# Kernel optimization log

Hardware: AMD Instinct MI355X
Metric: run time of the kernel (lower is better)

## Reference

```python
import jax, jax.numpy as jnp
import numpy as np

CONF_THRES = 0.25
IOU_THRES = 0.45
MAX_DET = 300
K_NMS = 2048          # static candidate cap for jit-compatible NMS
MAX_WH = 7680.0       # yolov5 class-offset trick for non-agnostic NMS
IN_H, IN_W = 640.0, 640.0     # network input size (self.size)
OUT_H, OUT_W = 1080.0, 1920.0  # original frame size (h, w)


def setup_inputs() -> dict:
    key = jax.random.key(0)
    k1, k2, k3, k4 = jax.random.split(key, 4)
    bs, n, nc = 16, 25200, 80
    # realistic raw yolov5 head output: xywh in pixels, obj/cls in [0,1]
    xy = jax.random.uniform(k1, (bs, n, 2), jnp.float32) * 640.0
    wh = jax.random.uniform(k2, (bs, n, 2), jnp.float32) * 120.0 + 2.0
    obj = jax.random.uniform(k3, (bs, n, 1), jnp.float32)
    cls = jax.random.uniform(k4, (bs, n, nc), jnp.float32)
    preds = jnp.concatenate([xy, wh, obj, cls], axis=-1)  # [bs, 25200, 85]
    return {"preds": preds}


def _xywh2xyxy(x):
    xy, wh = x[..., :2], x[..., 2:4]
    return jnp.concatenate([xy - wh * 0.5, xy + wh * 0.5], axis=-1)


def _iou_one_many(b, boxes):
    # b: [4], boxes: [K,4] (xyxy) -> [K]
    lt = jnp.maximum(b[:2], boxes[:, :2])
    rb = jnp.minimum(b[2:], boxes[:, 2:])
    wh = jnp.clip(rb - lt, 0.0)
    inter = wh[:, 0] * wh[:, 1]
    a1 = (b[2] - b[0]) * (b[3] - b[1])
    a2 = (boxes[:, 2] - boxes[:, 0]) * (boxes[:, 3] - boxes[:, 1])
    return inter / (a1 + a2 - inter + 1e-7)


def _nms_sorted(boxes, valid):
    # boxes [K,4] sorted by score desc (class-offset applied); valid [K] bool
    K = boxes.shape[0]
    idxs = jnp.arange(K)

    def step(suppressed, i):
        keep_i = valid[i] & jnp.logical_not(suppressed[i])
        iou = _iou_one_many(boxes[i], boxes)  # [K]
        suppressed = suppressed | (keep_i & (iou > IOU_THRES) & (idxs > i))
        return suppressed, keep_i

    _, keep = jax.lax.scan(step, jnp.zeros((K,), bool), idxs)
    # first MAX_DET kept indices (stable: preserves score order)
    sel = jnp.argsort(jnp.logical_not(keep), stable=True)[:MAX_DET]
    return sel, keep[sel]


def reference(preds):
    # --- yolov5 non_max_suppression (multi_label=False, agnostic=False) ---
    obj = preds[..., 4:5]                      # [bs,N,1]
    cls_conf = preds[..., 5:] * obj            # conf = obj * cls
    conf = jnp.max(cls_conf, axis=-1)          # [bs,N]
    cls = jnp.argmax(cls_conf, axis=-1)        # [bs,N] int
    mask = (preds[..., 4] > CONF_THRES) & (conf > CONF_THRES)
    score = jnp.where(mask, conf, -1.0)

    top_s, top_i = jax.lax.top_k(score, K_NMS)                      # [bs,K]
    cand_xywh = jnp.take_along_axis(preds[..., :4], top_i[..., None], axis=1)
    cand_boxes = _xywh2xyxy(cand_xywh)                              # [bs,K,4]
    cand_cls = jnp.take_along_axis(cls, top_i, axis=1)              # [bs,K]
    valid = top_s > 0.0

    boxes_off = cand_boxes + cand_cls[..., None].astype(cand_boxes.dtype) * MAX_WH
    sel, keep = jax.vmap(_nms_sorted)(boxes_off, valid)             # [bs,MAX_DET]

    det_boxes = jnp.take_along_axis(cand_boxes, sel[..., None], axis=1)
    det_scores = jnp.take_along_axis(top_s, sel, axis=1)
    det_cls = jnp.take_along_axis(cand_cls, sel, axis=1)

    # --- scale_bbox: (640,640) -> (h,w) original frame ---
    scale = jnp.array([OUT_W / IN_W, OUT_H / IN_H, OUT_W / IN_W, OUT_H / IN_H],
                      dtype=det_boxes.dtype)
    det_boxes = det_boxes * scale

    det = jnp.concatenate(
        [det_boxes, det_scores[..., None], det_cls[..., None].astype(det_boxes.dtype)],
        axis=-1)                                                    # [bs,MAX_DET,6]
    det = jnp.where(keep[..., None], det, 0.0)
    return det
```

## Files before the change

### kernel.cpp

```cpp
#include <hip/hip_runtime.h>
#include <stdint.h>

#define BS 16
#define NP 25200
#define NC 80
#define DIM 85
#define KN 2048
#define CAP 4096
#define BINS 512
#define MAXD 300
#define SBLK 99
#define QCAP 128

__global__ __launch_bounds__(256) void score_hist_kernel(const float* __restrict__ preds,
        float* __restrict__ score, int* __restrict__ clsout, int* __restrict__ hpart) {
    int b = blockIdx.x / SBLK;
    int chunk = blockIdx.x % SBLK;
    int tid = threadIdx.x;
    __shared__ int h[BINS];
    h[tid] = 0; h[tid + 256] = 0;
    __syncthreads();
    int n = chunk * 256 + tid;
    if (n < NP) {
        const float* bp = preds + ((size_t)b * NP + n) * DIM;
        float obj = bp[4];
        float sc = -1.0f; int bidx = 0;
        if (obj > 0.25f) {
            float best = -1.0f;
            #pragma unroll
            for (int kk = 0; kk < 10; ++kk) {
                float v[8];
                #pragma unroll
                for (int j = 0; j < 8; ++j) v[j] = bp[5 + kk * 8 + j];
                #pragma unroll
                for (int j = 0; j < 8; ++j) {
                    float s = v[j] * obj;
                    if (s > best) { best = s; bidx = kk * 8 + j; }
                }
            }
            if (best > 0.25f) sc = best;
        }
        int gi = b * NP + n;
        score[gi] = sc;
        clsout[gi] = bidx;
        if (sc > 0.0f) {
            int bin = (int)(__float_as_uint(sc) >> 15) - 0x7D00;
            bin = max(0, min(BINS - 1, bin));
            atomicAdd(&h[bin], 1);
        }
    }
    __syncthreads();
    int* hp = hpart + ((size_t)(b * SBLK + chunk)) * BINS;
    hp[tid] = h[tid];
    hp[tid + 256] = h[tid + 256];
}

template<int V, bool DESC, typename T>
__device__ inline void wave_bitonic(T (&v)[V], int lane) {
    const int N = V * 64;
    #pragma unroll
    for (int k = 2; k <= N; k <<= 1) {
        #pragma unroll
        for (int j = N >> 1; j > 0; j >>= 1) {
            if (j >= k) continue;
            if (j >= 64) {
                int dv = j >> 6;
                #pragma unroll
                for (int a = 0; a < V; ++a) {
                    int p = a ^ dv;
                    if (a < p) {
                        int e = a * 64;
                        bool kml = (((e & k) == 0) == DESC);
                        T lo = v[a], hi = v[p];
                        T mx = lo > hi ? lo : hi;
                        T mn = lo > hi ? hi : lo;
                        v[a] = kml ? mx : mn;
                        v[p] = kml ? mn : mx;
                    }
                }
            } else {
                #pragma unroll
                for (int a = 0; a < V; ++a) {
                    int e = a * 64 + lane;
                    T pv = __shfl_xor(v[a], j);
                    bool isLower = (lane & j) == 0;
                    bool kml = (((e & k) == 0) == DESC);
                    bool takeMax = (kml == isLower);
                    T mx = v[a] > pv ? v[a] : pv;
                    T mn = v[a] > pv ? pv : v[a];
                    v[a] = takeMax ? mx : mn;
                }
            }
        }
    }
}

__global__ __launch_bounds__(1024) void sort16_kernel(const float* __restrict__ score,
        const int* __restrict__ hpart,
        unsigned long long* __restrict__ gkeys, int* __restrict__ gmeta,
        int* __restrict__ gbstart, int* __restrict__ gcnt,
        unsigned char* __restrict__ carrU8, unsigned char* __restrict__ keepG) {
    int b = blockIdx.x;
    int tid = threadIdx.x;
    int lane = tid & 63;
    __shared__ int h[BINS];
    __shared__ int bstartA[BINS];
    __shared__ int bcnt[BINS];
    __shared__ int sT;
    if (tid < BINS) {
        int s = 0;
        const int* hp = hpart + ((size_t)b * SBLK) * BINS + tid;
        for (int c = 0; c < SBLK; ++c) s += hp[c * BINS];
        h[tid] = s;
        bcnt[tid] = 0;
    }
    __syncthreads();
    if (tid < 64) {
        int base = lane * 8;
        int v[8]; int ssum = 0;
        #pragma unroll
        for (int kk = 0; kk < 8; ++kk) { v[kk] = h[base + kk]; ssum += v[kk]; }
        int x = ssum;
        #pragma unroll
        for (int off = 1; off < 64; off <<= 1) {
            int y = __shfl_down(x, off);
            if (lane + off < 64) x += y;
        }
        int run = x - ssum;
        int cand = -1;
        #pragma unroll
        for (int kk = 7; kk >= 0; --kk) {
            bstartA[base + kk] = run;
            run += v[kk];
            if (run >= KN && cand < 0) cand = base + kk;
        }
        #pragma unroll
        for (int off = 1; off < 64; off <<= 1) cand = max(cand, __shfl_xor(cand, off));
        if (lane == 0) sT = max(cand, 0);
    }
    __syncthreads();
    int T = sT;
    int n = min(bstartA[T] + h[T], CAP);
    int Mb = min(n, KN);
    const float* sb = score + (size_t)b * NP;
    for (int i = tid; i < NP; i += 1024) {
        float sc = sb[i];
        if (sc > 0.0f) {
            int bin = (int)(__float_as_uint(sc) >> 15) - 0x7D00;
            bin = max(0, min(BINS - 1, bin));
            if (bin >= T) {
                int pos = bstartA[bin] + atomicAdd(&bcnt[bin], 1);
                if (pos < CAP) {
                    unsigned int ii = (unsigned int)i;
                    gkeys[(size_t)b * CAP + pos] =
                        ((unsigned long long)__float_as_uint(sc) << 32)
                        | (unsigned int)(~ii);
                }
            }
        }
    }
    for (int r = tid; r < KN; r += 1024) { keepG[b * KN + r] = 0; carrU8[b * KN + r] = 0xFF; }
    if (tid < BINS) { gbstart[b * BINS + tid] = bstartA[tid]; gcnt[b * BINS + tid] = h[tid]; }
    if (tid == 0) { gmeta[2 * b] = T; gmeta[2 * b + 1] = Mb; }
}

__global__ __launch_bounds__(256) void binsort_build_kernel(const float* __restrict__ preds,
        const int* __restrict__ cls, unsigned long long* __restrict__ gkeys,
        const int* __restrict__ gmeta, const int* __restrict__ gbstart,
        const int* __restrict__ gcnt,
        float4* __restrict__ gboxes, unsigned char* __restrict__ carrU8) {
    int b = blockIdx.x >> 5;
    int g = blockIdx.x & 31;
    int lane = threadIdx.x & 63;
    int wv = threadIdx.x >> 6;
    int T = gmeta[2 * b];
    int Mb = gmeta[2 * b + 1];
    int wslot = g * 4 + wv;
    for (int bin = T + wslot; bin < BINS; bin += 128) {
        int cnt = gcnt[b * BINS + bin];
        if (cnt <= 0) continue;
        int bs = gbstart[b * BINS + bin];
        if (bs >= Mb) continue;
        unsigned long long v[4];
        #pragma unroll
        for (int a = 0; a < 4; ++a) {
            int idx = a * 64 + lane;
            v[a] = (idx < cnt && bs + idx < CAP) ? gkeys[(size_t)b * CAP + bs + idx] : 0ull;
        }
        wave_bitonic<4, true>(v, lane);
        #pragma unroll
        for (int a = 0; a < 4; ++a) {
            int idx = a * 64 + lane;
            if (idx < cnt && bs + idx < CAP) gkeys[(size_t)b * CAP + bs + idx] = v[a];
        }
        #pragma unroll
        for (int a = 0; a < 4; ++a) {
            int idx = a * 64 + lane;
            int r = bs + idx;
            if (idx < cnt && r < Mb) {
                unsigned long long key = v[a];
                unsigned int i = ~(unsigned int)key;
                const float* p = preds + ((size_t)b * NP + i) * DIM;
                float x = p[0], y = p[1], w = p[2], hh = p[3];
                gboxes[b * KN + r] = make_float4(x - w * 0.5f, y - hh * 0.5f,
                                                x + w * 0.5f, y + hh * 0.5f);
                carrU8[b * KN + r] = (unsigned char)cls[(size_t)b * NP + i];
            }
        }
    }
}

__global__ __launch_bounds__(64) void nms_kernel(const float4* __restrict__ gboxes,
        const unsigned char* __restrict__ carrU8, const int* __restrict__ gmeta,
        unsigned char* __restrict__ keepG) {
    int b = blockIdx.x / NC;
    int c = blockIdx.x % NC;
    int lane = threadIdx.x;
    int Mb = gmeta[2 * b + 1];
    __shared__ unsigned short q[QCAP];
    int base = 0;
    for (int r0 = 0; r0 < Mb; r0 += 64) {
        int r = r0 + lane;
        bool mine = (r < Mb) && (carrU8[b * KN + r] == (unsigned char)c);
        unsigned long long m = __ballot(mine);
        int pos = base + (int)__popcll(m & ((1ull << lane) - 1ull));
        if (mine && pos < QCAP) q[pos] = (unsigned short)r;
        base += (int)__popcll(m);
    }
    __syncthreads();
    int nc = min(base, QCAP);
    if (nc <= 0) return;
    int ord0 = (lane < nc) ? (int)q[lane] : 0;
    int ord1 = (lane + 64 < nc) ? (int)q[64 + lane] : 0;
    float4 A0 = (lane < nc) ? gboxes[b * KN + ord0] : make_float4(0.f, 0.f, 0.f, 0.f);
    float4 A1 = (lane + 64 < nc) ? gboxes[b * KN + ord1] : make_float4(0.f, 0.f, 0.f, 0.f);
    float off = (float)c * 7680.0f;
    A0.x += off; A0.y += off; A0.z += off; A0.w += off;
    A1.x += off; A1.y += off; A1.z += off; A1.w += off;
    float ar0 = (A0.z - A0.x) * (A0.w - A0.y);
    float ar1 = (A1.z - A1.x) * (A1.w - A1.y);
    unsigned long long sup0 = 0, sup1 = 0, keep0 = 0, keep1 = 0;
    for (int idx = 0; idx < nc; ++idx) {
        bool hi = idx >= 64;
        int bit = idx & 63;
        unsigned long long s = hi ? sup1 : sup0;
        if ((s >> bit) & 1ull) continue;
        if (hi) keep1 |= 1ull << bit; else keep0 |= 1ull << bit;
        float bx_ = hi ? __shfl(A1.x, bit) : __shfl(A0.x, bit);
        float by_ = hi ? __shfl(A1.y, bit) : __shfl(A0.y, bit);
        float bz_ = hi ? __shfl(A1.z, bit) : __shfl(A0.z, bit);
        float bw_ = hi ? __shfl(A1.w, bit) : __shfl(A0.w, bit);
        float ba_ = hi ? __shfl(ar1, bit) : __shfl(ar0, bit);
        bool s0, s1;
        {
            float lx = fmaxf(bx_, A0.x), ly = fmaxf(by_, A0.y);
            float rx = fminf(bz_, A0.z), ry = fminf(bw_, A0.w);
            float iw = fmaxf(rx - lx, 0.0f), ih = fmaxf(ry - ly, 0.0f);
            float inter = iw * ih;
            float iou = inter / (ba_ + ar0 - inter + 1e-7f);
            s0 = (lane > idx) && (lane < nc) && (iou > 0.45f);
        }
        {
            float lx = fmaxf(bx_, A1.x), ly = fmaxf(by_, A1.y);
            float rx = fminf(bz_, A1.z), ry = fminf(bw_, A1.w);
            float iw = fmaxf(rx - lx, 0.0f), ih = fmaxf(ry - ly, 0.0f);
            float inter = iw * ih;
            float iou = inter / (ba_ + ar1 - inter + 1e-7f);
            s1 = ((64 + lane) > idx) && ((64 + lane) < nc) && (iou > 0.45f);
        }
        sup0 |= __ballot(s0);
        sup1 |= __ballot(s1);
    }
    if (lane < nc && ((keep0 >> lane) & 1ull)) keepG[b * KN + ord0] = 1;
    if (lane + 64 < nc && ((keep1 >> lane) & 1ull)) keepG[b * KN + ord1] = 1;
}

__global__ __launch_bounds__(64) void out_kernel(const unsigned char* __restrict__ keepG,
        const unsigned long long* __restrict__ gkeys, const float4* __restrict__ gboxes,
        const unsigned char* __restrict__ carrU8, float* __restrict__ out) {
    int b = blockIdx.x;
    int lane = threadIdx.x;
    int running = 0;
    for (int ch = 0; ch < 32; ++ch) {
        int r = ch * 64 + lane;
        bool kp = keepG[b * KN + r] != 0;
        unsigned long long m = __ballot(kp);
        int pos = running + (int)__popcll(m & ((1ull << lane) - 1ull));
        if (kp && pos < MAXD) {
            float4 bx = gboxes[b * KN + r];
            float sc = __uint_as_float((unsigned int)(gkeys[(size_t)b * CAP + r] >> 32));
            float* o = out + ((size_t)b * MAXD + pos) * 6;
            o[0] = bx.x * 3.0f;
            o[1] = bx.y * 1.6875f;
            o[2] = bx.z * 3.0f;
            o[3] = bx.w * 1.6875f;
            o[4] = sc;
            o[5] = (float)carrU8[b * KN + r];
        }
        running += (int)__popcll(m);
    }
}

extern "C" void kernel_launch(void* const* d_in, const int* in_sizes, int n_in,
                              void* d_out, int out_size, void* d_ws, size_t ws_size,
                              hipStream_t stream) {
    const float* preds = (const float*)d_in[0];
    float* out = (float*)d_out;
    char* ws = (char*)d_ws;
    size_t off = 0;
    auto alloc = [&](size_t bytes) -> void* {
        void* p = ws + off;
        off += (bytes + 255) & ~(size_t)255;
        return p;
    };
    float* score = (float*)alloc((size_t)BS * NP * 4);
    int* cls    = (int*)alloc((size_t)BS * NP * 4);
    int* hpart  = (int*)alloc((size_t)BS * SBLK * BINS * 4);
    unsigned long long* gkeys = (unsigned long long*)alloc((size_t)BS * CAP * 8);
    float4* gboxes = (float4*)alloc((size_t)BS * KN * 16);
    unsigned char* carrU8 = (unsigned char*)alloc((size_t)BS * KN);
    unsigned char* keepG  = (unsigned char*)alloc((size_t)BS * KN);
    int* gmeta   = (int*)alloc(BS * 2 * 4);
    int* gbstart = (int*)alloc((size_t)BS * BINS * 4);
    int* gcnt    = (int*)alloc((size_t)BS * BINS * 4);
    if (ws_size < off) return;

    hipMemsetAsync(d_out, 0, (size_t)out_size * 4, stream);

    score_hist_kernel<<<BS * SBLK, 256, 0, stream>>>(preds, score, cls, hpart);
    sort16_kernel<<<BS, 1024, 0, stream>>>(score, hpart, gkeys, gmeta, gbstart, gcnt,
                                           carrU8, keepG);
    binsort_build_kernel<<<BS * 32, 256, 0, stream>>>(preds, cls, gkeys, gmeta,
                                                      gbstart, gcnt, gboxes, carrU8);
    nms_kernel<<<BS * NC, 64, 0, stream>>>(gboxes, carrU8, gmeta, keepG);
    out_kernel<<<BS, 64, 0, stream>>>(keepG, gkeys, gboxes, carrU8, out);
}
```

Baseline: 262.5 us.

## Stage preds tiles through LDS and parallelize threshold scatter across blocks

The score/histogram kernel now loads contiguous 64-box tiles of preds into shared memory as coalesced float4 reads with double buffering, and splits each box's 80-class argmax across 4 lanes with shuffle reduction. The former single-block-per-batch sort16 kernel is split into a small threshold kernel, which also converts per-block histograms into per-block scatter offsets, and a 2048-block scatter kernel. This targets the uncoalesced strided preds reads and the serial 25200-element scan per batch, at the cost of one extra kernel launch and large shared-memory usage per block.

```diff
diff --git a/kernel.cpp b/kernel.cpp
--- a/kernel.cpp
+++ b/kernel.cpp
@@ -9,50 +9,180 @@
 #define CAP 4096
 #define BINS 512
 #define MAXD 300
-#define SBLK 99
+#define SCB 128
 #define QCAP 128
 
 __global__ __launch_bounds__(256) void score_hist_kernel(const float* __restrict__ preds,
         float* __restrict__ score, int* __restrict__ clsout, int* __restrict__ hpart) {
-    int b = blockIdx.x / SBLK;
-    int chunk = blockIdx.x % SBLK;
+    int b = blockIdx.x >> 7;
+    int blk = blockIdx.x & 127;
     int tid = threadIdx.x;
+    __shared__ float4 sbuf[2][1360];
     __shared__ int h[BINS];
     h[tid] = 0; h[tid + 256] = 0;
-    __syncthreads();
-    int n = chunk * 256 + tid;
-    if (n < NP) {
-        const float* bp = preds + ((size_t)b * NP + n) * DIM;
-        float obj = bp[4];
-        float sc = -1.0f; int bidx = 0;
-        if (obj > 0.25f) {
-            float best = -1.0f;
+    int g0  = (blk < 10) ? blk * 4 : blk * 3 + 10;
+    int cnt = (blk < 10) ? 4 : 3;
+    {
+        const float4* p4 = (const float4*)(preds + ((size_t)b * NP + (size_t)g0 * 64) * DIM);
+        int nb = min(64, NP - g0 * 64);
+        int tot4 = (nb * DIM) >> 2;
+        #pragma unroll
+        for (int kx = 0; kx < 6; ++kx) {
+            int idx = kx * 256 + tid;
+            if (idx < tot4) sbuf[0][idx] = p4[idx];
+        }
+    }
+    __syncthreads();
+    float4 tmp[6];
+    for (int i = 0; i < cnt; ++i) {
+        int tot4n = 0;
+        if (i + 1 < cnt) {
+            int g1 = g0 + i + 1;
+            int nb1 = min(64, NP - g1 * 64);
+            tot4n = (nb1 * DIM) >> 2;
+            const float4* p4 = (const float4*)(preds + ((size_t)b * NP + (size_t)g1 * 64) * DIM);
             #pragma unroll
-            for (int kk = 0; kk < 10; ++kk) {
-                float v[8];
-                #pragma unroll
-                for (int j = 0; j < 8; ++j) v[j] = bp[5 + kk * 8 + j];
-                #pragma unroll
-                for (int j = 0; j < 8; ++j) {
-                    float s = v[j] * obj;
-                    if (s > best) { best = s; bidx = kk * 8 + j; }
+            for (int kx = 0; kx < 6; ++kx) {
+                int idx = kx * 256 + tid;
+                tmp[kx] = (idx < tot4n) ? p4[idx] : make_float4(0.f, 0.f, 0.f, 0.f);
+            }
+        }
+        int gg = g0 + i;
+        int nb = min(64, NP - gg * 64);
+        const float* s = (const float*)sbuf[i & 1];
+        int box = tid >> 2, sub = tid & 3;
+        if (box < nb) {
+            const float* bp = s + box * DIM;
+            float obj = bp[4];
+            float best = -1.0f; int bidx = sub * 20;
+            #pragma unroll
+            for (int c = 0; c < 20; ++c) {
+                float v = bp[5 + sub * 20 + c] * obj;
+                if (v > best) { best = v; bidx = sub * 20 + c; }
+            }
+            #pragma unroll
+            for (int off = 1; off < 4; off <<= 1) {
+                float ob = __shfl_xor(best, off);
+                int   oi = __shfl_xor(bidx, off);
+                if (ob > best || (ob == best && oi < bidx)) { best = ob; bidx = oi; }
+            }
+            if (sub == 0) {
+                bool m = (obj > 0.25f) && (best > 0.25f);
+                float sc = m ? best : -1.0f;
+                int gidx = b * NP + gg * 64 + box;
+                score[gidx] = sc;
+                clsout[gidx] = bidx;
+                if (sc > 0.0f) {
+                    int bin = (int)(__float_as_uint(sc) >> 15) - 0x7D00;
+                    bin = max(0, min(BINS - 1, bin));
+                    atomicAdd(&h[bin], 1);
                 }
             }
-            if (best > 0.25f) sc = best;
-        }
-        int gi = b * NP + n;
-        score[gi] = sc;
-        clsout[gi] = bidx;
+        }
+        __syncthreads();
+        if (i + 1 < cnt) {
+            #pragma unroll
+            for (int kx = 0; kx < 6; ++kx) {
+                int idx = kx * 256 + tid;
+                if (idx < tot4n) sbuf[(i + 1) & 1][idx] = tmp[kx];
+            }
+            __syncthreads();
+        }
+    }
+    int* hp = hpart + ((size_t)(b * SCB + blk)) * BINS;
+    hp[tid] = h[tid];
+    hp[tid + 256] = h[tid + 256];
+}
+
+__global__ __launch_bounds__(512) void thresh_kernel(int* __restrict__ hpart,
+        int* __restrict__ gmeta, int* __restrict__ gbstart, int* __restrict__ gcnt,
+        unsigned char* __restrict__ carrU8, unsigned char* __restrict__ keepG) {
+    int b = blockIdx.x;
+    int tid = threadIdx.x;
+    int lane = tid & 63;
+    __shared__ int h[BINS];
+    __shared__ int bstartA[BINS];
+    __shared__ int sT;
+    int* hp = hpart + (size_t)b * SCB * BINS;
+    int s = 0;
+    for (int c = 0; c < SCB; ++c) s += hp[c * BINS + tid];
+    h[tid] = s;
+    __syncthreads();
+    if (tid < 64) {
+        int base = lane * 8;
+        int v[8]; int ssum = 0;
+        #pragma unroll
+        for (int kk = 0; kk < 8; ++kk) { v[kk] = h[base + kk]; ssum += v[kk]; }
+        int x = ssum;
+        #pragma unroll
+        for (int off = 1; off < 64; off <<= 1) {
+            int y = __shfl_down(x, off);
+            if (lane + off < 64) x += y;
+        }
+        int run = x - ssum;
+        int cand = -1;
+        #pragma unroll
+        for (int kk = 7; kk >= 0; --kk) {
+            bstartA[base + kk] = run;
+            run += v[kk];
+            if (run >= KN && cand < 0) cand = base + kk;
+        }
+        #pragma unroll
+        for (int off = 1; off < 64; off <<= 1) cand = max(cand, __shfl_xor(cand, off));
+        if (lane == 0) sT = max(cand, 0);
+    }
+    __syncthreads();
+    int T = sT;
+    int run = bstartA[tid];
+    for (int c = 0; c < SCB; ++c) {
+        int t = hp[c * BINS + tid];
+        hp[c * BINS + tid] = run;
+        run += t;
+    }
+    gbstart[b * BINS + tid] = bstartA[tid];
+    gcnt[b * BINS + tid] = h[tid];
+    if (tid == 0) {
+        int n = min(bstartA[T] + h[T], CAP);
+        gmeta[2 * b] = T;
+        gmeta[2 * b + 1] = min(n, KN);
+    }
+    for (int r = tid; r < KN; r += 512) { keepG[b * KN + r] = 0; carrU8[b * KN + r] = 0xFF; }
+}
+
+__global__ __launch_bounds__(256) void scatter_kernel(const float* __restrict__ score,
+        const int* __restrict__ hpart, const int* __restrict__ gmeta,
+        unsigned long long* __restrict__ gkeys) {
+    int b = blockIdx.x >> 7;
+    int blk = blockIdx.x & 127;
+    int tid = threadIdx.x;
+    __shared__ int basep[BINS];
+    __shared__ int cntL[BINS];
+    const int* hp = hpart + (size_t)(b * SCB + blk) * BINS;
+    basep[tid] = hp[tid]; basep[tid + 256] = hp[tid + 256];
+    cntL[tid] = 0; cntL[tid + 256] = 0;
+    __syncthreads();
+    int T = gmeta[2 * b];
+    int g0  = (blk < 10) ? blk * 4 : blk * 3 + 10;
+    int cntg = (blk < 10) ? 4 : 3;
+    int r0 = g0 * 64;
+    int nrows = min(cntg * 64, NP - r0);
+    for (int r = tid; r < nrows; r += 256) {
+        int i = r0 + r;
+        float sc = score[b * NP + i];
         if (sc > 0.0f) {
             int bin = (int)(__float_as_uint(sc) >> 15) - 0x7D00;
             bin = max(0, min(BINS - 1, bin));
-            atomicAdd(&h[bin], 1);
-        }
-    }
-    __syncthreads();
-    int* hp = hpart + ((size_t)(b * SBLK + chunk)) * BINS;
-    hp[tid] = h[tid];
-    hp[tid + 256] = h[tid + 256];
+            if (bin >= T) {
+                int pos = basep[bin] + atomicAdd(&cntL[bin], 1);
+                if (pos < CAP) {
+                    unsigned int ii = (unsigned int)i;
+                    gkeys[(size_t)b * CAP + pos] =
+                        ((unsigned long long)__float_as_uint(sc) << 32)
+                        | (unsigned int)(~ii);
+                }
+            }
+        }
+    }
 }
 
 template<int V, bool DESC, typename T>
@@ -93,75 +223,6 @@
             }
         }
     }
-}
-
-__global__ __launch_bounds__(1024) void sort16_kernel(const float* __restrict__ score,
-        const int* __restrict__ hpart,
-        unsigned long long* __restrict__ gkeys, int* __restrict__ gmeta,
-        int* __restrict__ gbstart, int* __restrict__ gcnt,
-        unsigned char* __restrict__ carrU8, unsigned char* __restrict__ keepG) {
-    int b = blockIdx.x;
-    int tid = threadIdx.x;
-    int lane = tid & 63;
-    __shared__ int h[BINS];
-    __shared__ int bstartA[BINS];
-    __shared__ int bcnt[BINS];
-    __shared__ int sT;
-    if (tid < BINS) {
-        int s = 0;
-        const int* hp = hpart + ((size_t)b * SBLK) * BINS + tid;
-        for (int c = 0; c < SBLK; ++c) s += hp[c * BINS];
-        h[tid] = s;
-        bcnt[tid] = 0;
-    }
-    __syncthreads();
-    if (tid < 64) {
-        int base = lane * 8;
-        int v[8]; int ssum = 0;
-        #pragma unroll
-        for (int kk = 0; kk < 8; ++kk) { v[kk] = h[base + kk]; ssum += v[kk]; }
-        int x = ssum;
-        #pragma unroll
-        for (int off = 1; off < 64; off <<= 1) {
-            int y = __shfl_down(x, off);
-            if (lane + off < 64) x += y;
-        }
-        int run = x - ssum;
-        int cand = -1;
-        #pragma unroll
-        for (int kk = 7; kk >= 0; --kk) {
-            bstartA[base + kk] = run;
-            run += v[kk];
-            if (run >= KN && cand < 0) cand = base + kk;
-        }
-        #pragma unroll
-        for (int off = 1; off < 64; off <<= 1) cand = max(cand, __shfl_xor(cand, off));
-        if (lane == 0) sT = max(cand, 0);
-    }
-    __syncthreads();
-    int T = sT;
-    int n = min(bstartA[T] + h[T], CAP);
-    int Mb = min(n, KN);
-    const float* sb = score + (size_t)b * NP;
-    for (int i = tid; i < NP; i += 1024) {
-        float sc = sb[i];
-        if (sc > 0.0f) {
-            int bin = (int)(__float_as_uint(sc) >> 15) - 0x7D00;
-            bin = max(0, min(BINS - 1, bin));
-            if (bin >= T) {
-                int pos = bstartA[bin] + atomicAdd(&bcnt[bin], 1);
-                if (pos < CAP) {
-                    unsigned int ii = (unsigned int)i;
-                    gkeys[(size_t)b * CAP + pos] =
-                        ((unsigned long long)__float_as_uint(sc) << 32)
-                        | (unsigned int)(~ii);
-                }
-            }
-        }
-    }
-    for (int r = tid; r < KN; r += 1024) { keepG[b * KN + r] = 0; carrU8[b * KN + r] = 0xFF; }
-    if (tid < BINS) { gbstart[b * BINS + tid] = bstartA[tid]; gcnt[b * BINS + tid] = h[tid]; }
-    if (tid == 0) { gmeta[2 * b] = T; gmeta[2 * b + 1] = Mb; }
 }
 
 __global__ __launch_bounds__(256) void binsort_build_kernel(const float* __restrict__ preds,
@@ -315,7 +376,7 @@
     };
     float* score = (float*)alloc((size_t)BS * NP * 4);
     int* cls    = (int*)alloc((size_t)BS * NP * 4);
-    int* hpart  = (int*)alloc((size_t)BS * SBLK * BINS * 4);
+    int* hpart  = (int*)alloc((size_t)BS * SCB * BINS * 4);
     unsigned long long* gkeys = (unsigned long long*)alloc((size_t)BS * CAP * 8);
     float4* gboxes = (float4*)alloc((size_t)BS * KN * 16);
     unsigned char* carrU8 = (unsigned char*)alloc((size_t)BS * KN);
@@ -327,9 +388,9 @@
 
     hipMemsetAsync(d_out, 0, (size_t)out_size * 4, stream);
 
-    score_hist_kernel<<<BS * SBLK, 256, 0, stream>>>(preds, score, cls, hpart);
-    sort16_kernel<<<BS, 1024, 0, stream>>>(score, hpart, gkeys, gmeta, gbstart, gcnt,
-                                           carrU8, keepG);
+    score_hist_kernel<<<BS * SCB, 256, 0, stream>>>(preds, score, cls, hpart);
+    thresh_kernel<<<BS, 512, 0, stream>>>(hpart, gmeta, gbstart, gcnt, carrU8, keepG);
+    scatter_kernel<<<BS * SCB, 256, 0, stream>>>(score, hpart, gmeta, gkeys);
     binsort_build_kernel<<<BS * 32, 256, 0, stream>>>(preds, cls, gkeys, gmeta,
                                                       gbstart, gcnt, gboxes, carrU8);
     nms_kernel<<<BS * NC, 64, 0, stream>>>(gboxes, carrU8, gmeta, keepG);
```

New measurement: 256.9 us. -2.1%, faster.

## Fuse sort, box build, NMS and output into one per-batch LDS kernel

Applied to the files above, without the earlier changes.

Four per-batch kernels (bin scatter, per-bin bitonic sort plus box gather, per-class NMS, output compaction) become one 1024-thread block per image. All keys, boxes, classes and keep flags now live in shared memory. Each of the 16 waves handles five classes' NMS in turn. The separate memset of the output is dropped; the kernel zeroes only the unused tail rows. This removes several launches and the global-memory round trips between stages. In exchange, binsort and NMS run on 16 blocks instead of hundreds, so much less of the GPU is used during those phases, and the block needs a large LDS footprint.

```diff
diff --git a/kernel.cpp b/kernel.cpp
--- a/kernel.cpp
+++ b/kernel.cpp
@@ -95,25 +95,32 @@
     }
 }
 
-__global__ __launch_bounds__(1024) void sort16_kernel(const float* __restrict__ score,
-        const int* __restrict__ hpart,
-        unsigned long long* __restrict__ gkeys, int* __restrict__ gmeta,
-        int* __restrict__ gbstart, int* __restrict__ gcnt,
-        unsigned char* __restrict__ carrU8, unsigned char* __restrict__ keepG) {
+__global__ __launch_bounds__(1024) void tail_kernel(const float* __restrict__ score,
+        const float* __restrict__ preds, const int* __restrict__ cls,
+        const int* __restrict__ hpart, float* __restrict__ out) {
     int b = blockIdx.x;
     int tid = threadIdx.x;
     int lane = tid & 63;
+    int wid = tid >> 6;
+
+    __shared__ unsigned long long k[CAP];
+    __shared__ float4 bx4[KN];
+    __shared__ unsigned char carr[KN];
+    __shared__ unsigned char keep[KN];
+    __shared__ unsigned short q[16][QCAP];
     __shared__ int h[BINS];
     __shared__ int bstartA[BINS];
     __shared__ int bcnt[BINS];
-    __shared__ int sT;
+    __shared__ int sT, sMb, sKept;
+
     if (tid < BINS) {
         int s = 0;
-        const int* hp = hpart + ((size_t)b * SBLK) * BINS + tid;
+        const int* hp = hpart + (size_t)b * SBLK * BINS + tid;
         for (int c = 0; c < SBLK; ++c) s += hp[c * BINS];
         h[tid] = s;
         bcnt[tid] = 0;
     }
+    for (int r = tid; r < KN; r += 1024) { carr[r] = 0xFF; keep[r] = 0; }
     __syncthreads();
     if (tid < 64) {
         int base = lane * 8;
@@ -139,9 +146,14 @@
         if (lane == 0) sT = max(cand, 0);
     }
     __syncthreads();
+    if (tid == 0) {
+        int T = sT;
+        int n = min(bstartA[T] + h[T], CAP);
+        sMb = min(n, KN);
+    }
+    __syncthreads();
     int T = sT;
-    int n = min(bstartA[T] + h[T], CAP);
-    int Mb = min(n, KN);
+    int Mb = sMb;
     const float* sb = score + (size_t)b * NP;
     for (int i = tid; i < NP; i += 1024) {
         float sc = sb[i];
@@ -152,46 +164,29 @@
                 int pos = bstartA[bin] + atomicAdd(&bcnt[bin], 1);
                 if (pos < CAP) {
                     unsigned int ii = (unsigned int)i;
-                    gkeys[(size_t)b * CAP + pos] =
-                        ((unsigned long long)__float_as_uint(sc) << 32)
-                        | (unsigned int)(~ii);
+                    k[pos] = ((unsigned long long)__float_as_uint(sc) << 32)
+                           | (unsigned int)(~ii);
                 }
             }
         }
     }
-    for (int r = tid; r < KN; r += 1024) { keepG[b * KN + r] = 0; carrU8[b * KN + r] = 0xFF; }
-    if (tid < BINS) { gbstart[b * BINS + tid] = bstartA[tid]; gcnt[b * BINS + tid] = h[tid]; }
-    if (tid == 0) { gmeta[2 * b] = T; gmeta[2 * b + 1] = Mb; }
-}
-
-__global__ __launch_bounds__(256) void binsort_build_kernel(const float* __restrict__ preds,
-        const int* __restrict__ cls, unsigned long long* __restrict__ gkeys,
-        const int* __restrict__ gmeta, const int* __restrict__ gbstart,
-        const int* __restrict__ gcnt,
-        float4* __restrict__ gboxes, unsigned char* __restrict__ carrU8) {
-    int b = blockIdx.x >> 5;
-    int g = blockIdx.x & 31;
-    int lane = threadIdx.x & 63;
-    int wv = threadIdx.x >> 6;
-    int T = gmeta[2 * b];
-    int Mb = gmeta[2 * b + 1];
-    int wslot = g * 4 + wv;
-    for (int bin = T + wslot; bin < BINS; bin += 128) {
-        int cnt = gcnt[b * BINS + bin];
+    __syncthreads();
+    for (int bin = T + wid; bin < BINS; bin += 16) {
+        int cnt = h[bin];
         if (cnt <= 0) continue;
-        int bs = gbstart[b * BINS + bin];
+        int bs = bstartA[bin];
         if (bs >= Mb) continue;
         unsigned long long v[4];
         #pragma unroll
         for (int a = 0; a < 4; ++a) {
             int idx = a * 64 + lane;
-            v[a] = (idx < cnt && bs + idx < CAP) ? gkeys[(size_t)b * CAP + bs + idx] : 0ull;
+            v[a] = (idx < cnt && bs + idx < CAP) ? k[bs + idx] : 0ull;
         }
         wave_bitonic<4, true>(v, lane);
         #pragma unroll
         for (int a = 0; a < 4; ++a) {
             int idx = a * 64 + lane;
-            if (idx < cnt && bs + idx < CAP) gkeys[(size_t)b * CAP + bs + idx] = v[a];
+            if (idx < cnt && bs + idx < CAP) k[bs + idx] = v[a];
         }
         #pragma unroll
         for (int a = 0; a < 4; ++a) {
@@ -202,103 +197,100 @@
                 unsigned int i = ~(unsigned int)key;
                 const float* p = preds + ((size_t)b * NP + i) * DIM;
                 float x = p[0], y = p[1], w = p[2], hh = p[3];
-                gboxes[b * KN + r] = make_float4(x - w * 0.5f, y - hh * 0.5f,
-                                                x + w * 0.5f, y + hh * 0.5f);
-                carrU8[b * KN + r] = (unsigned char)cls[(size_t)b * NP + i];
-            }
-        }
-    }
-}
-
-__global__ __launch_bounds__(64) void nms_kernel(const float4* __restrict__ gboxes,
-        const unsigned char* __restrict__ carrU8, const int* __restrict__ gmeta,
-        unsigned char* __restrict__ keepG) {
-    int b = blockIdx.x / NC;
-    int c = blockIdx.x % NC;
-    int lane = threadIdx.x;
-    int Mb = gmeta[2 * b + 1];
-    __shared__ unsigned short q[QCAP];
-    int base = 0;
-    for (int r0 = 0; r0 < Mb; r0 += 64) {
-        int r = r0 + lane;
-        bool mine = (r < Mb) && (carrU8[b * KN + r] == (unsigned char)c);
-        unsigned long long m = __ballot(mine);
-        int pos = base + (int)__popcll(m & ((1ull << lane) - 1ull));
-        if (mine && pos < QCAP) q[pos] = (unsigned short)r;
-        base += (int)__popcll(m);
-    }
-    __syncthreads();
-    int nc = min(base, QCAP);
-    if (nc <= 0) return;
-    int ord0 = (lane < nc) ? (int)q[lane] : 0;
-    int ord1 = (lane + 64 < nc) ? (int)q[64 + lane] : 0;
-    float4 A0 = (lane < nc) ? gboxes[b * KN + ord0] : make_float4(0.f, 0.f, 0.f, 0.f);
-    float4 A1 = (lane + 64 < nc) ? gboxes[b * KN + ord1] : make_float4(0.f, 0.f, 0.f, 0.f);
-    float off = (float)c * 7680.0f;
-    A0.x += off; A0.y += off; A0.z += off; A0.w += off;
-    A1.x += off; A1.y += off; A1.z += off; A1.w += off;
-    float ar0 = (A0.z - A0.x) * (A0.w - A0.y);
-    float ar1 = (A1.z - A1.x) * (A1.w - A1.y);
-    unsigned long long sup0 = 0, sup1 = 0, keep0 = 0, keep1 = 0;
-    for (int idx = 0; idx < nc; ++idx) {
-        bool hi = idx >= 64;
-        int bit = idx & 63;
-        unsigned long long s = hi ? sup1 : sup0;
-        if ((s >> bit) & 1ull) continue;
-        if (hi) keep1 |= 1ull << bit; else keep0 |= 1ull << bit;
-        float bx_ = hi ? __shfl(A1.x, bit) : __shfl(A0.x, bit);
-        float by_ = hi ? __shfl(A1.y, bit) : __shfl(A0.y, bit);
-        float bz_ = hi ? __shfl(A1.z, bit) : __shfl(A0.z, bit);
-        float bw_ = hi ? __shfl(A1.w, bit) : __shfl(A0.w, bit);
-        float ba_ = hi ? __shfl(ar1, bit) : __shfl(ar0, bit);
-        bool s0, s1;
-        {
-            float lx = fmaxf(bx_, A0.x), ly = fmaxf(by_, A0.y);
-            float rx = fminf(bz_, A0.z), ry = fminf(bw_, A0.w);
-            float iw = fmaxf(rx - lx, 0.0f), ih = fmaxf(ry - ly, 0.0f);
-            float inter = iw * ih;
-            float iou = inter / (ba_ + ar0 - inter + 1e-7f);
-            s0 = (lane > idx) && (lane < nc) && (iou > 0.45f);
-        }
-        {
-            float lx = fmaxf(bx_, A1.x), ly = fmaxf(by_, A1.y);
-            float rx = fminf(bz_, A1.z), ry = fminf(bw_, A1.w);
-            float iw = fmaxf(rx - lx, 0.0f), ih = fmaxf(ry - ly, 0.0f);
-            float inter = iw * ih;
-            float iou = inter / (ba_ + ar1 - inter + 1e-7f);
-            s1 = ((64 + lane) > idx) && ((64 + lane) < nc) && (iou > 0.45f);
-        }
-        sup0 |= __ballot(s0);
-        sup1 |= __ballot(s1);
-    }
-    if (lane < nc && ((keep0 >> lane) & 1ull)) keepG[b * KN + ord0] = 1;
-    if (lane + 64 < nc && ((keep1 >> lane) & 1ull)) keepG[b * KN + ord1] = 1;
-}
-
-__global__ __launch_bounds__(64) void out_kernel(const unsigned char* __restrict__ keepG,
-        const unsigned long long* __restrict__ gkeys, const float4* __restrict__ gboxes,
-        const unsigned char* __restrict__ carrU8, float* __restrict__ out) {
-    int b = blockIdx.x;
-    int lane = threadIdx.x;
-    int running = 0;
-    for (int ch = 0; ch < 32; ++ch) {
-        int r = ch * 64 + lane;
-        bool kp = keepG[b * KN + r] != 0;
-        unsigned long long m = __ballot(kp);
-        int pos = running + (int)__popcll(m & ((1ull << lane) - 1ull));
-        if (kp && pos < MAXD) {
-            float4 bx = gboxes[b * KN + r];
-            float sc = __uint_as_float((unsigned int)(gkeys[(size_t)b * CAP + r] >> 32));
-            float* o = out + ((size_t)b * MAXD + pos) * 6;
-            o[0] = bx.x * 3.0f;
-            o[1] = bx.y * 1.6875f;
-            o[2] = bx.z * 3.0f;
-            o[3] = bx.w * 1.6875f;
-            o[4] = sc;
-            o[5] = (float)carrU8[b * KN + r];
-        }
-        running += (int)__popcll(m);
-    }
+                bx4[r] = make_float4(x - w * 0.5f, y - hh * 0.5f,
+                                     x + w * 0.5f, y + hh * 0.5f);
+                carr[r] = (unsigned char)cls[(size_t)b * NP + i];
+            }
+        }
+    }
+    __syncthreads();
+    #pragma unroll
+    for (int t5 = 0; t5 < 5; ++t5) {
+        int c = wid + 16 * t5;
+        unsigned short* qw = q[wid];
+        int base = 0;
+        for (int r0 = 0; r0 < Mb; r0 += 64) {
+            int r = r0 + lane;
+            bool mine = (r < Mb) && (carr[r] == (unsigned char)c);
+            unsigned long long m = __ballot(mine);
+            int pos = base + (int)__popcll(m & ((1ull << lane) - 1ull));
+            if (mine && pos < QCAP) qw[pos] = (unsigned short)r;
+            base += (int)__popcll(m);
+        }
+        int nc = min(base, QCAP);
+        if (nc <= 0) continue;
+        int ord0 = (lane < nc) ? (int)qw[lane] : 0;
+        int ord1 = (lane + 64 < nc) ? (int)qw[64 + lane] : 0;
+        float4 A0 = (lane < nc) ? bx4[ord0] : make_float4(0.f, 0.f, 0.f, 0.f);
+        float4 A1 = (lane + 64 < nc) ? bx4[ord1] : make_float4(0.f, 0.f, 0.f, 0.f);
+        float off = (float)c * 7680.0f;
+        A0.x += off; A0.y += off; A0.z += off; A0.w += off;
+        A1.x += off; A1.y += off; A1.z += off; A1.w += off;
+        float ar0 = (A0.z - A0.x) * (A0.w - A0.y);
+        float ar1 = (A1.z - A1.x) * (A1.w - A1.y);
+        unsigned long long sup0 = 0, sup1 = 0, keep0 = 0, keep1 = 0;
+        for (int idx = 0; idx < nc; ++idx) {
+            bool hi = idx >= 64;
+            int bit = idx & 63;
+            unsigned long long s = hi ? sup1 : sup0;
+            if ((s >> bit) & 1ull) continue;
+            if (hi) keep1 |= 1ull << bit; else keep0 |= 1ull << bit;
+            float bx_ = hi ? __shfl(A1.x, bit) : __shfl(A0.x, bit);
+            float by_ = hi ? __shfl(A1.y, bit) : __shfl(A0.y, bit);
+            float bz_ = hi ? __shfl(A1.z, bit) : __shfl(A0.z, bit);
+            float bw_ = hi ? __shfl(A1.w, bit) : __shfl(A0.w, bit);
+            float ba_ = hi ? __shfl(ar1, bit) : __shfl(ar0, bit);
+            bool s0, s1;
+            {
+                float lx = fmaxf(bx_, A0.x), ly = fmaxf(by_, A0.y);
+                float rx = fminf(bz_, A0.z), ry = fminf(bw_, A0.w);
+                float iw = fmaxf(rx - lx, 0.0f), ih = fmaxf(ry - ly, 0.0f);
+                float inter = iw * ih;
+                float iou = inter / (ba_ + ar0 - inter + 1e-7f);
+                s0 = (lane > idx) && (lane < nc) && (iou > 0.45f);
+            }
+            {
+                float lx = fmaxf(bx_, A1.x), ly = fmaxf(by_, A1.y);
+                float rx = fminf(bz_, A1.z), ry = fminf(bw_, A1.w);
+                float iw = fmaxf(rx - lx, 0.0f), ih = fmaxf(ry - ly, 0.0f);
+                float inter = iw * ih;
+                float iou = inter / (ba_ + ar1 - inter + 1e-7f);
+                s1 = ((64 + lane) > idx) && ((64 + lane) < nc) && (iou > 0.45f);
+            }
+            sup0 |= __ballot(s0);
+            sup1 |= __ballot(s1);
+        }
+        if (lane < nc && ((keep0 >> lane) & 1ull)) keep[ord0] = 1;
+        if (lane + 64 < nc && ((keep1 >> lane) & 1ull)) keep[ord1] = 1;
+    }
+    __syncthreads();
+    if (tid < 64) {
+        int running = 0;
+        for (int ch = 0; ch < 32; ++ch) {
+            int r = ch * 64 + lane;
+            bool kp = keep[r] != 0;
+            unsigned long long m = __ballot(kp);
+            int pos = running + (int)__popcll(m & ((1ull << lane) - 1ull));
+            if (kp && pos < MAXD) {
+                float4 bx = bx4[r];
+                float sc = __uint_as_float((unsigned int)(k[r] >> 32));
+                float* o = out + ((size_t)b * MAXD + pos) * 6;
+                o[0] = bx.x * 3.0f;
+                o[1] = bx.y * 1.6875f;
+                o[2] = bx.z * 3.0f;
+                o[3] = bx.w * 1.6875f;
+                o[4] = sc;
+                o[5] = (float)carr[r];
+            }
+            running += (int)__popcll(m);
+        }
+        if (tid == 0) sKept = min(running, MAXD);
+    }
+    __syncthreads();
+    int kept = sKept;
+    int ztot = (MAXD - kept) * 6;
+    float* zbase = out + ((size_t)b * MAXD + kept) * 6;
+    for (int z = tid; z < ztot; z += 1024) zbase[z] = 0.0f;
 }
 
 extern "C" void kernel_launch(void* const* d_in, const int* in_sizes, int n_in,
@@ -316,22 +308,8 @@
     float* score = (float*)alloc((size_t)BS * NP * 4);
     int* cls    = (int*)alloc((size_t)BS * NP * 4);
     int* hpart  = (int*)alloc((size_t)BS * SBLK * BINS * 4);
-    unsigned long long* gkeys = (unsigned long long*)alloc((size_t)BS * CAP * 8);
-    float4* gboxes = (float4*)alloc((size_t)BS * KN * 16);
-    unsigned char* carrU8 = (unsigned char*)alloc((size_t)BS * KN);
-    unsigned char* keepG  = (unsigned char*)alloc((size_t)BS * KN);
-    int* gmeta   = (int*)alloc(BS * 2 * 4);
-    int* gbstart = (int*)alloc((size_t)BS * BINS * 4);
-    int* gcnt    = (int*)alloc((size_t)BS * BINS * 4);
     if (ws_size < off) return;
 
-    hipMemsetAsync(d_out, 0, (size_t)out_size * 4, stream);
-
     score_hist_kernel<<<BS * SBLK, 256, 0, stream>>>(preds, score, cls, hpart);
-    sort16_kernel<<<BS, 1024, 0, stream>>>(score, hpart, gkeys, gmeta, gbstart, gcnt,
-                                           carrU8, keepG);
-    binsort_build_kernel<<<BS * 32, 256, 0, stream>>>(preds, cls, gkeys, gmeta,
-                                                      gbstart, gcnt, gboxes, carrU8);
-    nms_kernel<<<BS * NC, 64, 0, stream>>>(gboxes, carrU8, gmeta, keepG);
-    out_kernel<<<BS, 64, 0, stream>>>(keepG, gkeys, gboxes, carrU8, out);
+    tail_kernel<<<BS, 1024, 0, stream>>>(score, preds, cls, hpart, out);
 }
```

New measurement: 357.7 us. 36.3% more time.
